# Kernel tuning notes

Hardware: AMD Instinct MI355X
Metric: run time of the kernel (lower is better)

## Reference

```python
import jax, jax.numpy as jnp
import numpy as np

FUTURE_K = 32
NEG_INF = -1e9  # finite large-negative to keep softmax NaN-free on fully-masked rows


def setup_inputs() -> dict:
    key = jax.random.key(0)
    hidden_states = jax.random.normal(key, (4, 2048, 1024), dtype=jnp.float32)
    return {"hidden_states": hidden_states}


def reference(hidden_states) -> jnp.ndarray:
    # Faithful vectorized version of FutureEncoder(summary_method='attention').
    # For each t: window = h[:, t+1 : min(t+1+K, S)], scores = h_t @ window^T,
    # summary_t = softmax(scores) @ window. t = S-1 (empty window) stays zero.
    B, S, D = hidden_states.shape
    offs = jnp.arange(1, FUTURE_K + 1)                 # [K]
    idx = jnp.arange(S)[:, None] + offs[None, :]       # [S, K] future indices t+1..t+K
    valid = idx < S                                     # [S, K]
    idx_c = jnp.minimum(idx, S - 1)
    fw = hidden_states[:, idx_c, :]                     # [B, S, K, D] gathered windows
    scores = jnp.einsum('bsd,bskd->bsk', hidden_states, fw)
    scores = jnp.where(valid[None, :, :], scores, NEG_INF)
    w = jax.nn.softmax(scores, axis=-1)                 # [B, S, K]
    w = jnp.where(valid[None, :, :], w, 0.0)
    out = jnp.einsum('bsk,bskd->bsd', w, fw)            # [B, S, D]
    any_valid = valid.any(axis=-1)                      # [S]; False only at t = S-1
    return jnp.where(any_valid[None, :, None], out, 0.0)
```

## Files before the change

### kernel.cpp

```cpp
#include <hip/hip_runtime.h>
#include <math.h>


constexpr int KF = 32;
constexpr int S_CONST = 2048;
constexpr int D_CONST = 1024;

__device__ inline float dot16(const float4* q, const float4* f) {
    float p = 0.f;
    #pragma unroll
    for (int c = 0; c < 4; ++c)
        p += q[c].x * f[c].x + q[c].y * f[c].y + q[c].z * f[c].z + q[c].w * f[c].w;
    return p;
}

__device__ inline float allreduce64(float p) {
    #pragma unroll
    for (int i = 1; i < 64; i <<= 1) p += __shfl_xor(p, i, 64);
    return p;
}

__device__ inline void upd(float4* a, float& m, float& l, float p, const float4* f) {
    float nm = fmaxf(m, p);
    float sc = __expf(m - nm);
    float e  = __expf(p - nm);
    m = nm;
    l = l * sc + e;
    #pragma unroll
    for (int c = 0; c < 4; ++c) {
        a[c].x = a[c].x * sc + e * f[c].x;
        a[c].y = a[c].y * sc + e * f[c].y;
        a[c].z = a[c].z * sc + e * f[c].z;
        a[c].w = a[c].w * sc + e * f[c].w;
    }
}

__global__ __launch_bounds__(256, 4)
void future_encoder_kernel(const float* __restrict__ h,
                           float* __restrict__ out,
                           int ntok) {
    int bid  = blockIdx.x;
    int nblk = gridDim.x;
    int lb   = bid;
    if ((nblk & 7) == 0) {
        int per = nblk >> 3;
        lb = (bid & 7) * per + (bid >> 3);
    }

    const int wave = threadIdx.x >> 6;
    const int lane = threadIdx.x & 63;
    const int pid  = lb * 4 + wave;
    const int t0   = pid * 2;
    if (t0 >= ntok) return;

    const int s0 = t0 & (S_CONST - 1);
    const size_t base0 = (size_t)t0 * D_CONST + lane * 4;
    const float* r0p = h + base0;

    float4 q0[4], q1[4];
    #pragma unroll
    for (int c = 0; c < 4; ++c) q0[c] = *(const float4*)(r0p + c * 256);
    #pragma unroll
    for (int c = 0; c < 4; ++c) q1[c] = *(const float4*)(r0p + D_CONST + c * 256);

    float4 a0[4] = {}, a1[4] = {};
    float m0 = -1e30f, l0 = 0.f, m1 = -1e30f, l1 = 0.f;

    const int jmax = min(33, (S_CONST - 1) - s0);

    {
        float p0 = allreduce64(dot16(q0, q1));
        upd(a0, m0, l0, p0, q1);
    }

    const int j2 = min(KF, jmax);
    const float* fp = r0p + 2 * D_CONST;
    #pragma unroll 2
    for (int j = 2; j <= j2; ++j, fp += D_CONST) {
        float4 f[4];
        #pragma unroll
        for (int c = 0; c < 4; ++c) f[c] = *(const float4*)(fp + c * 256);
        float p0 = dot16(q0, f);
        float p1 = dot16(q1, f);
        #pragma unroll
        for (int i = 1; i < 64; i <<= 1) {
            p0 += __shfl_xor(p0, i, 64);
            p1 += __shfl_xor(p1, i, 64);
        }
        upd(a0, m0, l0, p0, f);
        upd(a1, m1, l1, p1, f);
    }

    if (jmax >= 33) {
        float4 f[4];
        #pragma unroll
        for (int c = 0; c < 4; ++c) f[c] = *(const float4*)(fp + c * 256);
        float p1 = allreduce64(dot16(q1, f));
        upd(a1, m1, l1, p1, f);
    }

    const float inv0 = 1.0f / l0;
    const float inv1 = (jmax >= 2) ? (1.0f / l1) : 0.f;

    float* o0 = out + base0;
    #pragma unroll
    for (int c = 0; c < 4; ++c) {
        float4 r = {a0[c].x * inv0, a0[c].y * inv0, a0[c].z * inv0, a0[c].w * inv0};
        *(float4*)(o0 + c * 256) = r;
    }
    #pragma unroll
    for (int c = 0; c < 4; ++c) {
        float4 r = {a1[c].x * inv1, a1[c].y * inv1, a1[c].z * inv1, a1[c].w * inv1};
        *(float4*)(o0 + D_CONST + c * 256) = r;
    }
}

extern "C" void kernel_launch(void* const* d_in, const int* in_sizes, int n_in,
                              void* d_out, int out_size, void* d_ws, size_t ws_size,
                              hipStream_t stream) {
    const float* h = (const float*)d_in[0];
    float* out = (float*)d_out;
    const int ntok  = in_sizes[0] / D_CONST;
    const int pairs = (ntok + 1) / 2;
    const int blocks = (pairs + 3) / 4;
    future_encoder_kernel<<<blocks, 256, 0, stream>>>(h, out, ntok);
}
```

Measured before the change: 114.0 us.

## Compute window scores with split-bf16 MFMA over 16-token blocks and two-pass softmax

Replaces the per-pair online-softmax kernel with a block of 16 tokens per workgroup. Window scores for a 16x48 tile are computed with bf16 MFMA, using a hi/lo split (three products) to approximate fp32 accuracy, and each wave handles a 256-wide slice of D. The slices are reduced through LDS, followed by a softmax pass and a weighted-sum pass that reuses the overlapping window rows across 4 tokens per wave. The goal is fewer redundant loads of overlapping windows and moving the dot products onto matrix cores. The cost is an extra global re-read of the window rows in the sum pass, two block barriers, hardcoded token counts, and some loss of precision.

```diff
diff --git a/kernel.cpp b/kernel.cpp
--- a/kernel.cpp
+++ b/kernel.cpp
@@ -2,116 +2,179 @@
 #include <math.h>
 
 
-constexpr int KF = 32;
 constexpr int S_CONST = 2048;
-constexpr int D_CONST = 1024;
+constexpr int D = 1024;
+constexpr int G = 16;
+constexpr int NTOK = 8192;
+constexpr int JW = 48;
+constexpr int JP = 49;
 
-__device__ inline float dot16(const float4* q, const float4* f) {
-    float p = 0.f;
-    #pragma unroll
-    for (int c = 0; c < 4; ++c)
-        p += q[c].x * f[c].x + q[c].y * f[c].y + q[c].z * f[c].z + q[c].w * f[c].w;
-    return p;
+typedef short bf16x8 __attribute__((ext_vector_type(8)));
+typedef float f32x4  __attribute__((ext_vector_type(4)));
+
+__device__ inline unsigned short f2bf(float x) {
+    unsigned u = __builtin_bit_cast(unsigned, x);
+    u += 0x7fffu + ((u >> 16) & 1u);
+    return (unsigned short)(u >> 16);
+}
+__device__ inline float bf2f(unsigned short h) {
+    unsigned u = ((unsigned)h) << 16;
+    return __builtin_bit_cast(float, u);
 }
 
-__device__ inline float allreduce64(float p) {
+__device__ inline void cvt8(float4 x0, float4 x1, bf16x8& hi, bf16x8& lo) {
+    float xs[8] = {x0.x, x0.y, x0.z, x0.w, x1.x, x1.y, x1.z, x1.w};
     #pragma unroll
-    for (int i = 1; i < 64; i <<= 1) p += __shfl_xor(p, i, 64);
-    return p;
-}
-
-__device__ inline void upd(float4* a, float& m, float& l, float p, const float4* f) {
-    float nm = fmaxf(m, p);
-    float sc = __expf(m - nm);
-    float e  = __expf(p - nm);
-    m = nm;
-    l = l * sc + e;
-    #pragma unroll
-    for (int c = 0; c < 4; ++c) {
-        a[c].x = a[c].x * sc + e * f[c].x;
-        a[c].y = a[c].y * sc + e * f[c].y;
-        a[c].z = a[c].z * sc + e * f[c].z;
-        a[c].w = a[c].w * sc + e * f[c].w;
+    for (int e = 0; e < 8; ++e) {
+        unsigned short h = f2bf(xs[e]);
+        float hf = bf2f(h);
+        unsigned short l = f2bf(xs[e] - hf);
+        hi[e] = (short)h;
+        lo[e] = (short)l;
     }
 }
 
-__global__ __launch_bounds__(256, 4)
+__global__ __launch_bounds__(256, 2)
 void future_encoder_kernel(const float* __restrict__ h,
-                           float* __restrict__ out,
-                           int ntok) {
-    int bid  = blockIdx.x;
-    int nblk = gridDim.x;
-    int lb   = bid;
+                           float* __restrict__ out) {
+    __shared__ float sc[4 * G * JP];
+    __shared__ float wm[G * JP];
+
+    int bid = blockIdx.x, nblk = gridDim.x, lb = bid;
     if ((nblk & 7) == 0) {
         int per = nblk >> 3;
         lb = (bid & 7) * per + (bid >> 3);
     }
 
-    const int wave = threadIdx.x >> 6;
-    const int lane = threadIdx.x & 63;
-    const int pid  = lb * 4 + wave;
-    const int t0   = pid * 2;
-    if (t0 >= ntok) return;
-
-    const int s0 = t0 & (S_CONST - 1);
-    const size_t base0 = (size_t)t0 * D_CONST + lane * 4;
-    const float* r0p = h + base0;
-
-    float4 q0[4], q1[4];
-    #pragma unroll
-    for (int c = 0; c < 4; ++c) q0[c] = *(const float4*)(r0p + c * 256);
-    #pragma unroll
-    for (int c = 0; c < 4; ++c) q1[c] = *(const float4*)(r0p + D_CONST + c * 256);
-
-    float4 a0[4] = {}, a1[4] = {};
-    float m0 = -1e30f, l0 = 0.f, m1 = -1e30f, l1 = 0.f;
-
-    const int jmax = min(33, (S_CONST - 1) - s0);
+    const int tid  = threadIdx.x;
+    const int w    = tid >> 6;
+    const int lane = tid & 63;
+    const int t0   = lb * G;
+    const int s0   = t0 & (S_CONST - 1);
+    const int jlim = (S_CONST - 2) - s0;
 
     {
-        float p0 = allreduce64(dot16(q0, q1));
-        upd(a0, m0, l0, p0, q1);
+        const int d0   = w * 256;
+        const int mrow = lane & 15;
+        const int q8   = (lane >> 4) * 8;
+
+        const float* ap = h + (size_t)(t0 + mrow) * D + d0 + q8;
+        const float* bp0; const float* bp1; const float* bp2;
+        {
+            int r0 = min(t0 + 1 +  0 + mrow, NTOK - 1);
+            int r1 = min(t0 + 1 + 16 + mrow, NTOK - 1);
+            int r2 = min(t0 + 1 + 32 + mrow, NTOK - 1);
+            bp0 = h + (size_t)r0 * D + d0 + q8;
+            bp1 = h + (size_t)r1 * D + d0 + q8;
+            bp2 = h + (size_t)r2 * D + d0 + q8;
+        }
+
+        f32x4 acc[3] = {{0,0,0,0},{0,0,0,0},{0,0,0,0}};
+
+        #pragma unroll
+        for (int kk = 0; kk < 8; ++kk) {
+            const int o = kk * 32;
+            bf16x8 ah, al;
+            cvt8(*(const float4*)(ap + o), *(const float4*)(ap + o + 4), ah, al);
+
+            bf16x8 bh, bl;
+            cvt8(*(const float4*)(bp0 + o), *(const float4*)(bp0 + o + 4), bh, bl);
+            acc[0] = __builtin_amdgcn_mfma_f32_16x16x32_bf16(ah, bh, acc[0], 0, 0, 0);
+            acc[0] = __builtin_amdgcn_mfma_f32_16x16x32_bf16(ah, bl, acc[0], 0, 0, 0);
+            acc[0] = __builtin_amdgcn_mfma_f32_16x16x32_bf16(al, bh, acc[0], 0, 0, 0);
+
+            cvt8(*(const float4*)(bp1 + o), *(const float4*)(bp1 + o + 4), bh, bl);
+            acc[1] = __builtin_amdgcn_mfma_f32_16x16x32_bf16(ah, bh, acc[1], 0, 0, 0);
+            acc[1] = __builtin_amdgcn_mfma_f32_16x16x32_bf16(ah, bl, acc[1], 0, 0, 0);
+            acc[1] = __builtin_amdgcn_mfma_f32_16x16x32_bf16(al, bh, acc[1], 0, 0, 0);
+
+            cvt8(*(const float4*)(bp2 + o), *(const float4*)(bp2 + o + 4), bh, bl);
+            acc[2] = __builtin_amdgcn_mfma_f32_16x16x32_bf16(ah, bh, acc[2], 0, 0, 0);
+            acc[2] = __builtin_amdgcn_mfma_f32_16x16x32_bf16(ah, bl, acc[2], 0, 0, 0);
+            acc[2] = __builtin_amdgcn_mfma_f32_16x16x32_bf16(al, bh, acc[2], 0, 0, 0);
+        }
+
+        #pragma unroll
+        for (int t = 0; t < 3; ++t) {
+            #pragma unroll
+            for (int r = 0; r < 4; ++r) {
+                int m = (lane >> 4) * 4 + r;
+                int j = t * 16 + (lane & 15);
+                sc[(w * G + m) * JP + j] = acc[t][r];
+            }
+        }
     }
+    __syncthreads();
 
-    const int j2 = min(KF, jmax);
-    const float* fp = r0p + 2 * D_CONST;
-    #pragma unroll 2
-    for (int j = 2; j <= j2; ++j, fp += D_CONST) {
-        float4 f[4];
+    {
+        const int i   = tid >> 4;
+        const int sub = tid & 15;
+
+        float v[3];
         #pragma unroll
-        for (int c = 0; c < 4; ++c) f[c] = *(const float4*)(fp + c * 256);
-        float p0 = dot16(q0, f);
-        float p1 = dot16(q1, f);
+        for (int c = 0; c < 3; ++c) {
+            int j = sub + c * 16;
+            float s = sc[(0 * G + i) * JP + j] + sc[(1 * G + i) * JP + j]
+                    + sc[(2 * G + i) * JP + j] + sc[(3 * G + i) * JP + j];
+            bool valid = (j >= i) && (j <= i + 31) && (j <= jlim);
+            v[c] = valid ? s : -1e9f;
+        }
+        float mx = fmaxf(v[0], fmaxf(v[1], v[2]));
         #pragma unroll
-        for (int i = 1; i < 64; i <<= 1) {
-            p0 += __shfl_xor(p0, i, 64);
-            p1 += __shfl_xor(p1, i, 64);
+        for (int d = 1; d < 16; d <<= 1) mx = fmaxf(mx, __shfl_xor(mx, d, 16));
+
+        float e[3];
+        float sum = 0.f;
+        #pragma unroll
+        for (int c = 0; c < 3; ++c) { e[c] = __expf(v[c] - mx); sum += e[c]; }
+        #pragma unroll
+        for (int d = 1; d < 16; d <<= 1) sum += __shfl_xor(sum, d, 16);
+
+        const bool any = (mx > -5e8f);
+        const float inv = any ? (1.0f / sum) : 0.f;
+        #pragma unroll
+        for (int c = 0; c < 3; ++c) {
+            int j = sub + c * 16;
+            bool valid = (j >= i) && (j <= i + 31) && (j <= jlim);
+            wm[i * JP + j] = valid ? e[c] * inv : 0.f;
         }
-        upd(a0, m0, l0, p0, f);
-        upd(a1, m1, l1, p1, f);
     }
+    __syncthreads();
 
-    if (jmax >= 33) {
-        float4 f[4];
+    {
+        const int i0   = w * 4;
+        const int doff = lane * 4;
+        const int jhi  = min(min(i0 + 34, JW - 1), jlim);
+
+        float4 a0[4] = {}, a1[4] = {}, a2[4] = {}, a3[4] = {};
+
+        for (int j = i0; j <= jhi; ++j) {
+            float w0 = wm[(i0 + 0) * JP + j];
+            float w1 = wm[(i0 + 1) * JP + j];
+            float w2 = wm[(i0 + 2) * JP + j];
+            float w3 = wm[(i0 + 3) * JP + j];
+            if (w0 + w1 + w2 + w3 != 0.f) {
+                const float* fp = h + (size_t)(t0 + 1 + j) * D + doff;
+                #pragma unroll
+                for (int c = 0; c < 4; ++c) {
+                    float4 f = *(const float4*)(fp + c * 256);
+                    a0[c].x += w0 * f.x; a0[c].y += w0 * f.y; a0[c].z += w0 * f.z; a0[c].w += w0 * f.w;
+                    a1[c].x += w1 * f.x; a1[c].y += w1 * f.y; a1[c].z += w1 * f.z; a1[c].w += w1 * f.w;
+                    a2[c].x += w2 * f.x; a2[c].y += w2 * f.y; a2[c].z += w2 * f.z; a2[c].w += w2 * f.w;
+                    a3[c].x += w3 * f.x; a3[c].y += w3 * f.y; a3[c].z += w3 * f.z; a3[c].w += w3 * f.w;
+                }
+            }
+        }
+
+        float* o0 = out + (size_t)(t0 + i0) * D + doff;
         #pragma unroll
-        for (int c = 0; c < 4; ++c) f[c] = *(const float4*)(fp + c * 256);
-        float p1 = allreduce64(dot16(q1, f));
-        upd(a1, m1, l1, p1, f);
-    }
-
-    const float inv0 = 1.0f / l0;
-    const float inv1 = (jmax >= 2) ? (1.0f / l1) : 0.f;
-
-    float* o0 = out + base0;
-    #pragma unroll
-    for (int c = 0; c < 4; ++c) {
-        float4 r = {a0[c].x * inv0, a0[c].y * inv0, a0[c].z * inv0, a0[c].w * inv0};
-        *(float4*)(o0 + c * 256) = r;
-    }
-    #pragma unroll
-    for (int c = 0; c < 4; ++c) {
-        float4 r = {a1[c].x * inv1, a1[c].y * inv1, a1[c].z * inv1, a1[c].w * inv1};
-        *(float4*)(o0 + D_CONST + c * 256) = r;
+        for (int c = 0; c < 4; ++c) *(float4*)(o0 + 0 * D + c * 256) = a0[c];
+        #pragma unroll
+        for (int c = 0; c < 4; ++c) *(float4*)(o0 + 1 * D + c * 256) = a1[c];
+        #pragma unroll
+        for (int c = 0; c < 4; ++c) *(float4*)(o0 + 2 * D + c * 256) = a2[c];
+        #pragma unroll
+        for (int c = 0; c < 4; ++c) *(float4*)(o0 + 3 * D + c * 256) = a3[c];
     }
 }
 
@@ -120,8 +183,7 @@
                               hipStream_t stream) {
     const float* h = (const float*)d_in[0];
     float* out = (float*)d_out;
-    const int ntok  = in_sizes[0] / D_CONST;
-    const int pairs = (ntok + 1) / 2;
-    const int blocks = (pairs + 3) / 4;
-    future_encoder_kernel<<<blocks, 256, 0, stream>>>(h, out, ntok);
+    const int ntok = in_sizes[0] / D;
+    const int blocks = ntok / G;
+    future_encoder_kernel<<<blocks, 256, 0, stream>>>(h, out);
 }
```

Result: faster. 105.4 us (-7.5%).
